# Performance work log

Measured on AMD Instinct MI355X. Metric: run time of the kernel, lower is better.

## Reference

```python
import jax, jax.numpy as jnp
import numpy as np

RADIUS = 1
KS = 2 * RADIUS + 1  # kernel_size

def setup_inputs() -> dict:
    key = jax.random.key(0)
    k1, k2 = jax.random.split(key)
    shape = (1, 32, 96, 96, 96)  # [B, C, D, H, W]
    fixed = jax.random.normal(k1, shape, dtype=jnp.float32)
    moving = jax.random.normal(k2, shape, dtype=jnp.float32)
    return {"fixed": fixed, "moving": moving}

def reference(fixed, moving):
    # Local window correlation: out[b, idx, p] = sum_c fixed[b,c,p] * moving[b,c,p+off(idx)-radius]
    # with zero padding, matching the one-hot grouped conv3d in the torch module.
    B, C, D, H, W = fixed.shape
    pad = ((0, 0), (0, 0), (RADIUS, RADIUS), (RADIUS, RADIUS), (RADIUS, RADIUS))
    mp = jnp.pad(moving, pad)  # zero-padded moving
    corrs = []
    # Offsets enumerated in the same (i, j, k) row-major order as the torch module.
    for i in range(KS):
        for j in range(KS):
            for k in range(KS):
                shifted = mp[:, :, i:i + D, j:j + H, k:k + W]  # [B,C,D,H,W]
                corrs.append(jnp.sum(fixed * shifted, axis=1))  # reduce channels
    out = jnp.stack(corrs, axis=1)  # [B, kernel_volume, D, H, W]
    scale = jnp.asarray(C, fixed.dtype) ** -0.5  # normalize=True
    return out * scale
```

## Files before the change

kernel.cpp:

```cpp
#include <hip/hip_runtime.h>

#define N 96
#define NNN (N * N * N)
#define C_CH 32

#define TXD 8
#define TYD 8
#define TZD 4
#define VX 4
#define TW (TXD * VX)
#define TH TYD
#define TD TZD

#define HWS 35
#define HH 10
#define HD 6
#define PLANE (HWS * HH)
#define HTOT (PLANE * HD)
#define NTH (TXD * TYD * TZD)
#define NR ((HTOT + NTH - 1) / NTH)
#define SMSZ (NR * NTH)

typedef float vfloat4 __attribute__((ext_vector_type(4)));

__global__ __launch_bounds__(NTH, 2) void wincorr_kernel(
    const float* __restrict__ fixedp,
    const float* __restrict__ movingp,
    float* __restrict__ outp)
{
    __shared__ float smA[SMSZ];
    __shared__ float smB[SMSZ];

    const int tx = threadIdx.x;
    const int ty = threadIdx.y;
    const int tz = threadIdx.z;
    const int tid = tx + TXD * ty + TXD * TYD * tz;

    const int w0 = blockIdx.x * TW;
    const int h0 = blockIdx.y * TH;
    const int d0 = blockIdx.z * TD;

    int off[NR];
    int lwa[NR];
    #pragma unroll
    for (int r = 0; r < NR; ++r) {
        const int a = tid + r * NTH;
        const int z   = a / PLANE;
        const int rm  = a - z * PLANE;
        const int y   = rm / HWS;
        const int x   = rm - y * HWS;
        const int sd = d0 - 1 + z;
        const int sh = h0 - 1 + y;
        const int sw = w0 - 1 + x;
        const bool ok = (a < HTOT) && (x < TW + 2) &&
                        ((unsigned)sd < N) && ((unsigned)sh < N) && ((unsigned)sw < N);
        off[r] = ok ? ((sd * N + sh) * N + sw) : 0;
        lwa[r] = ok ? a : (HTOT + (tid & 63));
    }

    const int gw = w0 + VX * tx;
    const int fix_base = ((d0 + tz) * N + (h0 + ty)) * N + gw;
    const int lbase = tz * PLANE + ty * HWS + VX * tx;

    float acc[27][VX];
    #pragma unroll
    for (int s = 0; s < 27; ++s)
        #pragma unroll
        for (int v = 0; v < VX; ++v) acc[s][v] = 0.0f;

    float st0[NR], st1[NR];
    #pragma unroll
    for (int r = 0; r < NR; ++r) st0[r] = movingp[off[r]];
    {
        const float* m1 = movingp + (size_t)NNN;
        #pragma unroll
        for (int r = 0; r < NR; ++r) st1[r] = m1[off[r]];
    }
    float4 f0 = *(const float4*)&fixedp[fix_base];
    float4 f1 = *(const float4*)&fixedp[(size_t)NNN + fix_base];

    #pragma unroll
    for (int r = 0; r < NR; ++r) {
        smA[tid + r * NTH] = 0.0f;
        smB[tid + r * NTH] = 0.0f;
    }
    __syncthreads();

    auto step = [&](int c, float* __restrict__ smw, float (&st)[NR], float4& f) {
        #pragma unroll
        for (int r = 0; r < NR; ++r)
            smw[lwa[r]] = st[r];

        const float fv[VX] = {f.x, f.y, f.z, f.w};

        if (c + 2 < C_CH) {
            const float* mn = movingp + (size_t)(c + 2) * NNN;
            #pragma unroll
            for (int r = 0; r < NR; ++r) st[r] = mn[off[r]];
            f = *(const float4*)&fixedp[(size_t)(c + 2) * NNN + fix_base];
        }

        asm volatile("s_waitcnt lgkmcnt(0)" ::: "memory");
        __builtin_amdgcn_s_barrier();
        asm volatile("" ::: "memory");

        #pragma unroll
        for (int i = 0; i < 3; ++i) {
            #pragma unroll
            for (int j = 0; j < 3; ++j) {
                const float* row = &smw[lbase + i * PLANE + j * HWS];
                float wv[VX + 2];
                #pragma unroll
                for (int m = 0; m < VX + 2; ++m) wv[m] = row[m];
                #pragma unroll
                for (int k = 0; k < 3; ++k)
                    #pragma unroll
                    for (int v = 0; v < VX; ++v)
                        acc[(i * 3 + j) * 3 + k][v] += fv[v] * wv[v + k];
            }
        }
    };

    for (int c = 0; c < C_CH; c += 2) {
        step(c,     smA, st0, f0);
        step(c + 1, smB, st1, f1);
    }

    const float scale = 0.17677669529663687f;
    #pragma unroll
    for (int s = 0; s < 27; ++s) {
        vfloat4 o;
        o.x = acc[s][0] * scale;
        o.y = acc[s][1] * scale;
        o.z = acc[s][2] * scale;
        o.w = acc[s][3] * scale;
        __builtin_nontemporal_store(o, (vfloat4*)&outp[(size_t)s * NNN + fix_base]);
    }
}

extern "C" void kernel_launch(void* const* d_in, const int* in_sizes, int n_in,
                              void* d_out, int out_size, void* d_ws, size_t ws_size,
                              hipStream_t stream) {
    const float* fixedp  = (const float*)d_in[0];
    const float* movingp = (const float*)d_in[1];
    float* outp = (float*)d_out;

    dim3 block(TXD, TYD, TZD);
    dim3 grid(N / TW, N / TH, N / TD);
    wincorr_kernel<<<grid, block, 0, stream>>>(fixedp, movingp, outp);
}
```

Measured before the change: 282.9 us.

## Halve per-thread outputs to raise occupancy and mask halo writes arithmetically

Each thread now computes 2 outputs along W instead of 4, with 16 threads in x, so the block has 512 threads and launch bounds target 4 blocks per CU. The aim is a smaller accumulator register footprint and more resident waves to hide latency. Out-of-range halo elements are now zeroed by multiplying with a per-slot mask, which replaces the dummy-slot scatter and removes the initial shared-memory clear and its barrier. In exchange each thread gets less register reuse of window loads: it reads 4 LDS values per row for 2 outputs instead of 6 for 4, and fixed and output traffic uses float2 instead of float4.

```diff
diff --git a/kernel.cpp b/kernel.cpp
--- a/kernel.cpp
+++ b/kernel.cpp
@@ -4,10 +4,10 @@
 #define NNN (N * N * N)
 #define C_CH 32
 
-#define TXD 8
+#define TXD 16
 #define TYD 8
 #define TZD 4
-#define VX 4
+#define VX 2
 #define TW (TXD * VX)
 #define TH TYD
 #define TD TZD
@@ -21,9 +21,9 @@
 #define NR ((HTOT + NTH - 1) / NTH)
 #define SMSZ (NR * NTH)
 
-typedef float vfloat4 __attribute__((ext_vector_type(4)));
+typedef float vfloat2 __attribute__((ext_vector_type(2)));
 
-__global__ __launch_bounds__(NTH, 2) void wincorr_kernel(
+__global__ __launch_bounds__(NTH, 4) void wincorr_kernel(
     const float* __restrict__ fixedp,
     const float* __restrict__ movingp,
     float* __restrict__ outp)
@@ -40,8 +40,8 @@
     const int h0 = blockIdx.y * TH;
     const int d0 = blockIdx.z * TD;
 
-    int off[NR];
-    int lwa[NR];
+    int   off[NR];
+    float msk[NR];
     #pragma unroll
     for (int r = 0; r < NR; ++r) {
         const int a = tid + r * NTH;
@@ -55,7 +55,7 @@
         const bool ok = (a < HTOT) && (x < TW + 2) &&
                         ((unsigned)sd < N) && ((unsigned)sh < N) && ((unsigned)sw < N);
         off[r] = ok ? ((sd * N + sh) * N + sw) : 0;
-        lwa[r] = ok ? a : (HTOT + (tid & 63));
+        msk[r] = ok ? 1.0f : 0.0f;
     }
 
     const int gw = w0 + VX * tx;
@@ -76,28 +76,21 @@
         #pragma unroll
         for (int r = 0; r < NR; ++r) st1[r] = m1[off[r]];
     }
-    float4 f0 = *(const float4*)&fixedp[fix_base];
-    float4 f1 = *(const float4*)&fixedp[(size_t)NNN + fix_base];
+    float2 f0 = *(const float2*)&fixedp[fix_base];
+    float2 f1 = *(const float2*)&fixedp[(size_t)NNN + fix_base];
 
-    #pragma unroll
-    for (int r = 0; r < NR; ++r) {
-        smA[tid + r * NTH] = 0.0f;
-        smB[tid + r * NTH] = 0.0f;
-    }
-    __syncthreads();
-
-    auto step = [&](int c, float* __restrict__ smw, float (&st)[NR], float4& f) {
+    auto step = [&](int c, float* __restrict__ smw, float (&st)[NR], float2& f) {
         #pragma unroll
         for (int r = 0; r < NR; ++r)
-            smw[lwa[r]] = st[r];
+            smw[tid + r * NTH] = st[r] * msk[r];
 
-        const float fv[VX] = {f.x, f.y, f.z, f.w};
+        const float fv0 = f.x, fv1 = f.y;
 
         if (c + 2 < C_CH) {
             const float* mn = movingp + (size_t)(c + 2) * NNN;
             #pragma unroll
             for (int r = 0; r < NR; ++r) st[r] = mn[off[r]];
-            f = *(const float4*)&fixedp[(size_t)(c + 2) * NNN + fix_base];
+            f = *(const float2*)&fixedp[(size_t)(c + 2) * NNN + fix_base];
         }
 
         asm volatile("s_waitcnt lgkmcnt(0)" ::: "memory");
@@ -113,10 +106,10 @@
                 #pragma unroll
                 for (int m = 0; m < VX + 2; ++m) wv[m] = row[m];
                 #pragma unroll
-                for (int k = 0; k < 3; ++k)
-                    #pragma unroll
-                    for (int v = 0; v < VX; ++v)
-                        acc[(i * 3 + j) * 3 + k][v] += fv[v] * wv[v + k];
+                for (int k = 0; k < 3; ++k) {
+                    acc[(i * 3 + j) * 3 + k][0] += fv0 * wv[k];
+                    acc[(i * 3 + j) * 3 + k][1] += fv1 * wv[k + 1];
+                }
             }
         }
     };
@@ -129,12 +122,10 @@
     const float scale = 0.17677669529663687f;
     #pragma unroll
     for (int s = 0; s < 27; ++s) {
-        vfloat4 o;
+        vfloat2 o;
         o.x = acc[s][0] * scale;
         o.y = acc[s][1] * scale;
-        o.z = acc[s][2] * scale;
-        o.w = acc[s][3] * scale;
-        __builtin_nontemporal_store(o, (vfloat4*)&outp[(size_t)s * NNN + fix_base]);
+        __builtin_nontemporal_store(o, (vfloat2*)&outp[(size_t)s * NNN + fix_base]);
     }
 }
 
```

New measurement: 362.8 us. 28.3% more time.

## Give each wavefront a private LDS halo tile to eliminate block barriers

Applied to the files above, without the earlier changes.

Reorganizes the block so each of the four wavefronts computes its own 16x4x4 output sub-tile from a private double-buffered LDS halo. This removes the per-channel workgroup barrier and the LDS zero-init, and replaces out-of-bounds redirection with a multiply-by-mask. The trade-off is more redundant halo loads from global memory and reliance on intra-wave LDS ordering without explicit synchronization.

```diff
diff --git a/kernel.cpp b/kernel.cpp
--- a/kernel.cpp
+++ b/kernel.cpp
@@ -4,22 +4,12 @@
 #define NNN (N * N * N)
 #define C_CH 32
 
-#define TXD 8
-#define TYD 8
-#define TZD 4
-#define VX 4
-#define TW (TXD * VX)
-#define TH TYD
-#define TD TZD
-
-#define HWS 35
-#define HH 10
-#define HD 6
-#define PLANE (HWS * HH)
-#define HTOT (PLANE * HD)
-#define NTH (TXD * TYD * TZD)
-#define NR ((HTOT + NTH - 1) / NTH)
-#define SMSZ (NR * NTH)
+#define HWS 19
+#define HPLANE (HWS * 6)
+#define HTOT (HPLANE * 6)
+#define NR 11
+#define WBUF (NR * 64)
+#define NTH 256
 
 typedef float vfloat4 __attribute__((ext_vector_type(4)));
 
@@ -28,45 +18,48 @@
     const float* __restrict__ movingp,
     float* __restrict__ outp)
 {
-    __shared__ float smA[SMSZ];
-    __shared__ float smB[SMSZ];
+    __shared__ float sm[4][2][WBUF];
 
-    const int tx = threadIdx.x;
-    const int ty = threadIdx.y;
-    const int tz = threadIdx.z;
-    const int tid = tx + TXD * ty + TXD * TYD * tz;
+    const int tid  = threadIdx.x;
+    const int lane = tid & 63;
+    const int wid  = tid >> 6;
+    const int lx = lane & 3;
+    const int ly = (lane >> 2) & 3;
+    const int lz = lane >> 4;
 
-    const int w0 = blockIdx.x * TW;
-    const int h0 = blockIdx.y * TH;
-    const int d0 = blockIdx.z * TD;
+    const int w0 = blockIdx.x * 32 + (wid & 1) * 16;
+    const int h0 = blockIdx.y * 8  + (wid >> 1) * 4;
+    const int d0 = blockIdx.z * 4;
 
-    int off[NR];
-    int lwa[NR];
+    int   off[NR];
+    float msk[NR];
     #pragma unroll
     for (int r = 0; r < NR; ++r) {
-        const int a = tid + r * NTH;
-        const int z   = a / PLANE;
-        const int rm  = a - z * PLANE;
-        const int y   = rm / HWS;
-        const int x   = rm - y * HWS;
+        const int a  = lane + 64 * r;
+        const int z  = a / HPLANE;
+        const int rm = a - z * HPLANE;
+        const int y  = rm / HWS;
+        const int x  = rm - y * HWS;
         const int sd = d0 - 1 + z;
         const int sh = h0 - 1 + y;
         const int sw = w0 - 1 + x;
-        const bool ok = (a < HTOT) && (x < TW + 2) &&
+        const bool ok = (a < HTOT) && (x < 18) &&
                         ((unsigned)sd < N) && ((unsigned)sh < N) && ((unsigned)sw < N);
         off[r] = ok ? ((sd * N + sh) * N + sw) : 0;
-        lwa[r] = ok ? a : (HTOT + (tid & 63));
+        msk[r] = ok ? 1.0f : 0.0f;
     }
 
-    const int gw = w0 + VX * tx;
-    const int fix_base = ((d0 + tz) * N + (h0 + ty)) * N + gw;
-    const int lbase = tz * PLANE + ty * HWS + VX * tx;
+    const int fix_base = ((d0 + lz) * N + (h0 + ly)) * N + (w0 + 4 * lx);
+    const int lbase = lz * HPLANE + ly * HWS + 4 * lx;
 
-    float acc[27][VX];
+    float* const myA = &sm[wid][0][0];
+    float* const myB = &sm[wid][1][0];
+
+    float acc[27][4];
     #pragma unroll
     for (int s = 0; s < 27; ++s)
         #pragma unroll
-        for (int v = 0; v < VX; ++v) acc[s][v] = 0.0f;
+        for (int v = 0; v < 4; ++v) acc[s][v] = 0.0f;
 
     float st0[NR], st1[NR];
     #pragma unroll
@@ -79,19 +72,12 @@
     float4 f0 = *(const float4*)&fixedp[fix_base];
     float4 f1 = *(const float4*)&fixedp[(size_t)NNN + fix_base];
 
-    #pragma unroll
-    for (int r = 0; r < NR; ++r) {
-        smA[tid + r * NTH] = 0.0f;
-        smB[tid + r * NTH] = 0.0f;
-    }
-    __syncthreads();
-
     auto step = [&](int c, float* __restrict__ smw, float (&st)[NR], float4& f) {
         #pragma unroll
         for (int r = 0; r < NR; ++r)
-            smw[lwa[r]] = st[r];
+            smw[lane + 64 * r] = st[r] * msk[r];
 
-        const float fv[VX] = {f.x, f.y, f.z, f.w};
+        const float fv[4] = {f.x, f.y, f.z, f.w};
 
         if (c + 2 < C_CH) {
             const float* mn = movingp + (size_t)(c + 2) * NNN;
@@ -100,30 +86,27 @@
             f = *(const float4*)&fixedp[(size_t)(c + 2) * NNN + fix_base];
         }
 
-        asm volatile("s_waitcnt lgkmcnt(0)" ::: "memory");
-        __builtin_amdgcn_s_barrier();
-        asm volatile("" ::: "memory");
 
         #pragma unroll
         for (int i = 0; i < 3; ++i) {
             #pragma unroll
             for (int j = 0; j < 3; ++j) {
-                const float* row = &smw[lbase + i * PLANE + j * HWS];
-                float wv[VX + 2];
+                const float* row = &smw[lbase + i * HPLANE + j * HWS];
+                float wv[6];
                 #pragma unroll
-                for (int m = 0; m < VX + 2; ++m) wv[m] = row[m];
+                for (int m = 0; m < 6; ++m) wv[m] = row[m];
                 #pragma unroll
                 for (int k = 0; k < 3; ++k)
                     #pragma unroll
-                    for (int v = 0; v < VX; ++v)
+                    for (int v = 0; v < 4; ++v)
                         acc[(i * 3 + j) * 3 + k][v] += fv[v] * wv[v + k];
             }
         }
     };
 
     for (int c = 0; c < C_CH; c += 2) {
-        step(c,     smA, st0, f0);
-        step(c + 1, smB, st1, f1);
+        step(c,     myA, st0, f0);
+        step(c + 1, myB, st1, f1);
     }
 
     const float scale = 0.17677669529663687f;
@@ -145,7 +128,7 @@
     const float* movingp = (const float*)d_in[1];
     float* outp = (float*)d_out;
 
-    dim3 block(TXD, TYD, TZD);
-    dim3 grid(N / TW, N / TH, N / TD);
+    dim3 block(NTH, 1, 1);
+    dim3 grid(N / 32, N / 8, N / 4);
     wincorr_kernel<<<grid, block, 0, stream>>>(fixedp, movingp, outp);
 }
```

After: 327.4 us. +15.8%, slower.
